# Performance work log

Hardware: AMD Instinct MI355X
Metric: run time of the kernel (lower is better)

The kernel has to match this reference:

```python
import jax, jax.numpy as jnp
import numpy as np

B, T, H, F, E = 512, 32, 768, 3072, 3  # E = num_route_experts = num_experts - 1 (top-1 beam)


def setup_inputs() -> dict:
    key = jax.random.key(0)
    ks = jax.random.split(key, 4)
    s = 0.02
    return {
        "x": jax.random.normal(ks[0], (B, T, H), jnp.float32),
        "Wg": jax.random.normal(ks[1], (E, H), jnp.float32) * s,
        "W1": jax.random.normal(ks[2], (E, H, F), jnp.float32) * s,
        "b1": jnp.zeros((E, F), jnp.float32),
        "W2": jax.random.normal(ks[3], (E, F, H), jnp.float32) * s,
        "b2": jnp.zeros((E, H), jnp.float32),
    }


def reference(x, Wg, W1, b1, W2, b2):
    # forward_gate: mean-pool over tokens (attention_mask is all-ones), linear gate, softmax
    scores = jax.nn.softmax(jnp.mean(x, axis=1) @ Wg.T, axis=-1)  # [B, E]
    # beam_search, first layer with num_route_beam=1: plain top-1 expert selection
    _, idx = jax.lax.top_k(scores, 1)
    sel = idx[:, 0]  # [B] int32, selected expert per sample
    # forward_expert_ffn: densely run EVERY route expert (gelu MLP) on the full batch
    h = jax.nn.gelu(jnp.einsum('bth,ehf->betf', x, W1) + b1[None, :, None, :], approximate=False)  # [B,E,T,F]
    y = jnp.einsum('betf,efh->beth', h, W2) + b2[None, :, None, :]  # [B,E,T,H]
    # weight_type == 'ffn_prob': one-hot mask times gate prob, then sum over experts
    w = scores * jax.nn.one_hot(sel, E, dtype=scores.dtype)  # [B, E]
    out = jnp.einsum('beth,be->bth', y, w)  # [B, T, H]
    return out
```

## Files before the change

### kernel.cpp

```cpp
#include <hip/hip_runtime.h>
#include <hip/hip_bf16.h>
#include <cstdint>
#include <cstddef>

namespace {

constexpr int kB = 512, kT = 32, kH = 768, kF = 3072, kE = 3;
constexpr int kMaxTiles = 131;
constexpr int kMaxChunk = 131;
constexpr int kXPermTile = 128 * kH;
constexpr int kHbufTile  = 128 * kF;

typedef __attribute__((ext_vector_type(8))) short short8;
typedef __attribute__((ext_vector_type(4))) float f32x4;

__device__ __forceinline__ void gld_lds16(const void* g, void* l) {
  __builtin_amdgcn_global_load_lds(
      (const __attribute__((address_space(1))) void*)g,
      (__attribute__((address_space(3))) void*)l, 16, 0, 0);
}

__device__ __forceinline__ float bf2f(__hip_bfloat16 v) { return __bfloat162float(v); }
__device__ __forceinline__ unsigned short f2bfb(float f) {
  __hip_bfloat16 h = __float2bfloat16(f);
  return *reinterpret_cast<unsigned short*>(&h);
}

__global__ void k_sniff(const unsigned short* __restrict__ w, int nwords,
                        int* __restrict__ flag) {
  __shared__ int cnt_s;
  if (threadIdx.x == 0) cnt_s = 0;
  __syncthreads();
  int local = 0;
  for (int i = threadIdx.x; i < nwords; i += 256) {
    unsigned e = (w[i] >> 7) & 0xFF;
    if (e >= 0xC0) ++local;
  }
  atomicAdd(&cnt_s, local);
  __syncthreads();
  if (threadIdx.x == 0) *flag = (cnt_s > 64) ? 1 : 0;
}

__global__ void k_route(const void* __restrict__ xv, const void* __restrict__ Wgv,
                        const int* __restrict__ flagX, const int* __restrict__ flagG,
                        float* __restrict__ wsel,
                        int* __restrict__ cnt, int* __restrict__ lists) {
  bool fx = (*flagX != 0), fg = (*flagG != 0);
  const float* xf = (const float*)xv;
  const __hip_bfloat16* xb = (const __hip_bfloat16*)xv;
  const float* wf = (const float*)Wgv;
  const __hip_bfloat16* wb = (const __hip_bfloat16*)Wgv;
  int b = blockIdx.x;
  int tid = threadIdx.x;
  float a0 = 0.f, a1 = 0.f, a2 = 0.f;
  for (int h = tid; h < kH; h += 256) {
    size_t base = (size_t)b * kT * kH + h;
    float s = 0.f;
#pragma unroll
    for (int t = 0; t < kT; ++t) {
      size_t i = base + (size_t)t * kH;
      s += fx ? xf[i] : bf2f(xb[i]);
    }
    s *= (1.f / kT);
    a0 += s * (fg ? wf[0 * kH + h] : bf2f(wb[0 * kH + h]));
    a1 += s * (fg ? wf[1 * kH + h] : bf2f(wb[1 * kH + h]));
    a2 += s * (fg ? wf[2 * kH + h] : bf2f(wb[2 * kH + h]));
  }
  __shared__ float red[3][256];
  red[0][tid] = a0; red[1][tid] = a1; red[2][tid] = a2;
  __syncthreads();
  for (int s2 = 128; s2 > 0; s2 >>= 1) {
    if (tid < s2) {
      red[0][tid] += red[0][tid + s2];
      red[1][tid] += red[1][tid + s2];
      red[2][tid] += red[2][tid + s2];
    }
    __syncthreads();
  }
  if (tid == 0) {
    float l0 = red[0][0], l1 = red[1][0], l2 = red[2][0];
    int am = 0; float mx = l0;
    if (l1 > mx) { mx = l1; am = 1; }
    if (l2 > mx) { mx = l2; am = 2; }
    float e0 = expf(l0 - mx), e1 = expf(l1 - mx), e2 = expf(l2 - mx);
    float inv = 1.f / (e0 + e1 + e2);
    float sc = (am == 0 ? e0 : (am == 1 ? e1 : e2)) * inv;
    wsel[b] = sc;
    int pos = atomicAdd(&cnt[am], 1);
    lists[am * kB + pos] = b;
  }
}

__global__ void k_tiles(const int* __restrict__ cnt, const int* __restrict__ lists,
                        int* __restrict__ tileExpert, int* __restrict__ tileBatch,
                        int* __restrict__ numTiles) {
  if (threadIdx.x == 0 && blockIdx.x == 0) {
    int t = 0;
    for (int e = 0; e < kE; ++e) {
      int c = cnt[e];
      for (int i = 0; i < c; i += 4) {
        tileExpert[t] = e;
        for (int s = 0; s < 4; ++s)
          tileBatch[t * 4 + s] = (i + s < c) ? lists[e * kB + i + s] : -1;
        ++t;
      }
    }
    *numTiles = t;
    for (int tt = t; tt < kMaxTiles; ++tt) {
      tileExpert[tt] = 0;
      for (int s = 0; s < 4; ++s) tileBatch[tt * 4 + s] = -1;
    }
  }
}

__global__ __launch_bounds__(256)
void k_transpose(const void* __restrict__ srcv, __hip_bfloat16* __restrict__ dst_,
                 int K, int N, const int* __restrict__ flag) {
  bool f32 = (*flag != 0);
  const float* sf = (const float*)srcv;
  const unsigned short* sb = (const unsigned short*)srcv;
  unsigned short* dst = (unsigned short*)dst_;
  __shared__ __align__(16) unsigned short t[64][73];
  int e = blockIdx.z;
  int n0 = blockIdx.x * 64, k0 = blockIdx.y * 64;
  size_t eoff = (size_t)e * K * N;
  int tr = threadIdx.x >> 4;
  int tc4 = (threadIdx.x & 15) * 4;
#pragma unroll
  for (int i = 0; i < 4; ++i) {
    int r = tr + 16 * i;
    size_t idx = eoff + (size_t)(k0 + r) * N + n0 + tc4;
    if (f32) {
      float4 u = *(const float4*)(sf + idx);
      t[r][tc4] = f2bfb(u.x); t[r][tc4 + 1] = f2bfb(u.y);
      t[r][tc4 + 2] = f2bfb(u.z); t[r][tc4 + 3] = f2bfb(u.w);
    } else {
      ushort4 u = *(const ushort4*)(sb + idx);
      t[r][tc4] = u.x; t[r][tc4 + 1] = u.y; t[r][tc4 + 2] = u.z; t[r][tc4 + 3] = u.w;
    }
  }
  __syncthreads();
#pragma unroll
  for (int i = 0; i < 4; ++i) {
    int rn = tr + 16 * i;
    ushort4 v;
    v.x = t[tc4][rn]; v.y = t[tc4 + 1][rn]; v.z = t[tc4 + 2][rn]; v.w = t[tc4 + 3][rn];
    *(ushort4*)(dst + eoff + (size_t)(n0 + rn) * K + k0 + tc4) = v;
  }
}

__global__ __launch_bounds__(256)
void k_convert_x(const void* __restrict__ xv, const int* __restrict__ flagX,
                 const int* __restrict__ tileBatch, const int* __restrict__ numTiles,
                 __hip_bfloat16* __restrict__ xperm) {
  int tile = blockIdx.y;
  if (tile >= *numTiles) return;
  int kblk = blockIdx.x;
  bool fx = (*flagX != 0);
  const float* xf = (const float*)xv;
  const __hip_bfloat16* xb = (const __hip_bfloat16*)xv;
  int tb0 = tileBatch[tile * 4];
  int tb[4];
#pragma unroll
  for (int s = 0; s < 4; ++s) {
    int bb = tileBatch[tile * 4 + s];
    tb[s] = (bb < 0) ? tb0 : bb;
  }
  int tid = threadIdx.x;
  short8* dst = (short8*)(xperm + (size_t)tile * kXPermTile + kblk * 8192);
#pragma unroll
  for (int i = 0; i < 4; ++i) {
    int s = i * 256 + tid;
    int m = (s >> 2) & 127, kk = s >> 9;
    int q = (s & 3) ^ ((s >> 3) & 3);
    int row = tb[m >> 5] * kT + (m & 31);
    size_t src = (size_t)row * kH + kblk * 64 + kk * 32 + q * 8;
    short8 v;
    if (fx) {
      float4 u = *(const float4*)(xf + src);
      float4 w = *(const float4*)(xf + src + 4);
      v[0] = f2bfb(u.x); v[1] = f2bfb(u.y); v[2] = f2bfb(u.z); v[3] = f2bfb(u.w);
      v[4] = f2bfb(w.x); v[5] = f2bfb(w.y); v[6] = f2bfb(w.z); v[7] = f2bfb(w.w);
    } else {
      v = *(const short8*)(xb + src);
    }
    dst[s] = v;
  }
}

__global__ __launch_bounds__(256, 2)
void k_ffn1(const __hip_bfloat16* __restrict__ xperm,
            const __hip_bfloat16* __restrict__ w1t,
            const __hip_bfloat16* __restrict__ b1,
            const int* __restrict__ tileExpert,
            const int* __restrict__ numTiles,
            int tileOff,
            __hip_bfloat16* __restrict__ hbuf) {
  int j = blockIdx.y;
  int local = j / 3;
  int tile = local + tileOff;
  if (tile >= *numTiles) return;
  int nIdx = 8 * (j % 3) + blockIdx.x;
  int nbase = nIdx * 128;
  int e = tileExpert[tile];
  __shared__ __align__(16) short ldsA[8192];
  __shared__ __align__(16) short ldsB[8192];
  int tid = threadIdx.x;
  int lane = tid & 63, wid = tid >> 6;
  int wm = wid >> 1, wn = wid & 1;
  int lane16 = lane & 15, qf = lane >> 4;
  int swzl = (lane16 >> 1) & 3;
  int qx = (qf ^ swzl) * 8;

  f32x4 acc[4][4];
#pragma unroll
  for (int r = 0; r < 4; ++r)
#pragma unroll
    for (int c = 0; c < 4; ++c) acc[r][c] = (f32x4)0.f;

  const __hip_bfloat16* w1e = w1t + (size_t)e * kF * kH;
  const __hip_bfloat16* xtile = xperm + (size_t)tile * kXPermTile;
  const __hip_bfloat16* gB[4];
  short* lA[4];
  short* lB[4];
  int aoff[4];
#pragma unroll
  for (int it = 0; it < 4; ++it) {
    int s = it * 256 + tid;
    int m = (s >> 2) & 127, kk = s >> 9;
    int q = (s & 3) ^ ((s >> 3) & 3);
    aoff[it] = s * 8;
    gB[it] = w1e + (size_t)(nbase + m) * kH + kk * 32 + q * 8;
    lA[it] = &ldsA[s * 8];
    lB[it] = &ldsB[s * 8];
  }

  for (int k0 = 0; k0 < kH; k0 += 64) {
#pragma unroll
    for (int it = 0; it < 4; ++it) gld_lds16(xtile + k0 * 128 + aoff[it], lA[it]);
#pragma unroll
    for (int it = 0; it < 4; ++it) gld_lds16(gB[it] + k0, lB[it]);
    __syncthreads();
#pragma unroll
    for (int kk = 0; kk < 2; ++kk) {
      short8 af[4], bfr[4];
#pragma unroll
      for (int r = 0; r < 4; ++r) {
        int mr = wm * 64 + r * 16 + lane16;
        af[r] = *(const short8*)&ldsA[(kk * 512 + mr * 4) * 8 + qx];
      }
#pragma unroll
      for (int c = 0; c < 4; ++c) {
        int mb = wn * 64 + c * 16 + lane16;
        bfr[c] = *(const short8*)&ldsB[(kk * 512 + mb * 4) * 8 + qx];
      }
#pragma unroll
      for (int r = 0; r < 4; ++r)
#pragma unroll
        for (int c = 0; c < 4; ++c)
          acc[r][c] = __builtin_amdgcn_mfma_f32_16x16x32_bf16(af[r], bfr[c], acc[r][c], 0, 0, 0);
    }
    __syncthreads();
  }

  __hip_bfloat16* htile = hbuf + (size_t)local * kHbufTile;
  int q4 = qf * 4;
#pragma unroll
  for (int c = 0; c < 4; ++c) {
    int n = nbase + wn * 64 + c * 16 + lane16;
    int kblk2 = n >> 6, kkn = (n >> 5) & 1, qn = (n >> 3) & 3, jj = n & 7;
    float bias = bf2f(b1[e * kF + n]);
    __hip_bfloat16* hb = htile + kblk2 * 8192 + kkn * 4096 + jj;
#pragma unroll
    for (int r = 0; r < 4; ++r) {
#pragma unroll
      for (int g = 0; g < 4; ++g) {
        int m = wm * 64 + r * 16 + q4 + g;
        float v = acc[r][c][g] + bias;
        float ge = 0.5f * v * (1.f + erff(v * 0.70710678118654752f));
        hb[(m * 4 + (qn ^ ((m >> 1) & 3))) * 8] = __float2bfloat16(ge);
      }
    }
  }
}

__global__ __launch_bounds__(256, 2)
void k_ffn2(const __hip_bfloat16* __restrict__ hbuf,
            const __hip_bfloat16* __restrict__ w2t,
            const __hip_bfloat16* __restrict__ b2,
            const float* __restrict__ wsel,
            const int* __restrict__ tileExpert,
            const int* __restrict__ tileBatch,
            const int* __restrict__ numTiles,
            int tileOff, int chunk,
            float* __restrict__ out) {
  int j = blockIdx.y;
  int local = blockIdx.x + 8 * (j / 6);
  if (local >= chunk) return;
  int tile = local + tileOff;
  if (tile >= *numTiles) return;
  int nbase = (j % 6) * 128;
  int e = tileExpert[tile];
  int tbraw[4];
  float sc[4];
#pragma unroll
  for (int s = 0; s < 4; ++s) {
    int bb = tileBatch[tile * 4 + s];
    tbraw[s] = bb;
    sc[s] = (bb >= 0) ? wsel[bb] : 0.f;
  }
  __shared__ __align__(16) short ldsA[8192];
  __shared__ __align__(16) short ldsB[8192];
  int tid = threadIdx.x;
  int lane = tid & 63, wid = tid >> 6;
  int wm = wid >> 1, wn = wid & 1;
  int lane16 = lane & 15, qf = lane >> 4;
  int swzl = (lane16 >> 1) & 3;
  int qx = (qf ^ swzl) * 8;

  f32x4 acc[4][4];
#pragma unroll
  for (int r = 0; r < 4; ++r)
#pragma unroll
    for (int c = 0; c < 4; ++c) acc[r][c] = (f32x4)0.f;

  const __hip_bfloat16* w2e = w2t + (size_t)e * kF * kH;
  const __hip_bfloat16* htile = hbuf + (size_t)local * kHbufTile;
  const __hip_bfloat16* gB[4];
  short* lA[4];
  short* lB[4];
  int aoff[4];
#pragma unroll
  for (int it = 0; it < 4; ++it) {
    int s = it * 256 + tid;
    int m = (s >> 2) & 127, kk = s >> 9;
    int q = (s & 3) ^ ((s >> 3) & 3);
    aoff[it] = s * 8;
    gB[it] = w2e + (size_t)(nbase + m) * kF + kk * 32 + q * 8;
    lA[it] = &ldsA[s * 8];
    lB[it] = &ldsB[s * 8];
  }

  for (int k0 = 0; k0 < kF; k0 += 64) {
#pragma unroll
    for (int it = 0; it < 4; ++it) gld_lds16(htile + k0 * 128 + aoff[it], lA[it]);
#pragma unroll
    for (int it = 0; it < 4; ++it) gld_lds16(gB[it] + k0, lB[it]);
    __syncthreads();
#pragma unroll
    for (int kk = 0; kk < 2; ++kk) {
      short8 af[4], bfr[4];
#pragma unroll
      for (int r = 0; r < 4; ++r) {
        int mr = wm * 64 + r * 16 + lane16;
        af[r] = *(const short8*)&ldsA[(kk * 512 + mr * 4) * 8 + qx];
      }
#pragma unroll
      for (int c = 0; c < 4; ++c) {
        int mb = wn * 64 + c * 16 + lane16;
        bfr[c] = *(const short8*)&ldsB[(kk * 512 + mb * 4) * 8 + qx];
      }
#pragma unroll
      for (int r = 0; r < 4; ++r)
#pragma unroll
        for (int c = 0; c < 4; ++c)
          acc[r][c] = __builtin_amdgcn_mfma_f32_16x16x32_bf16(af[r], bfr[c], acc[r][c], 0, 0, 0);
    }
    __syncthreads();
  }

  int q4 = qf * 4;
#pragma unroll
  for (int c = 0; c < 4; ++c) {
    int ncol = wn * 64 + c * 16 + lane16;
    float bias = bf2f(b2[e * kH + nbase + ncol]);
#pragma unroll
    for (int r = 0; r < 4; ++r) {
      int s = (wm * 64 + r * 16) >> 5;
      int bb = tbraw[s];
      if (bb < 0) continue;
      float scale = sc[s];
#pragma unroll
      for (int g = 0; g < 4; ++g) {
        int m = wm * 64 + r * 16 + q4 + g;
        float v = (acc[r][c][g] + bias) * scale;
        out[((size_t)(bb * kT + (m & 31))) * kH + nbase + ncol] = v;
      }
    }
  }
}

}

extern "C" void kernel_launch(void* const* d_in, const int* in_sizes, int n_in,
                              void* d_out, int out_size, void* d_ws, size_t ws_size,
                              hipStream_t stream) {
  (void)in_sizes; (void)n_in; (void)out_size;
  float* out = (float*)d_out;

  char* ws = (char*)d_ws;
  size_t off = 0;
  auto alloc = [&](size_t bytes) -> char* {
    char* p = ws + off;
    off = (off + bytes + 255) & ~(size_t)255;
    return p;
  };
  int*   flagX      = (int*)alloc(4);
  int*   flagG      = (int*)alloc(4);
  int*   flagW1     = (int*)alloc(4);
  int*   flagW2     = (int*)alloc(4);
  int*   cnt        = (int*)alloc(kE * 4);
  float* wsel       = (float*)alloc(kB * 4);
  int*   lists      = (int*)alloc((size_t)kE * kB * 4);
  int*   tileExpert = (int*)alloc(kMaxTiles * 4);
  int*   tileBatch  = (int*)alloc(kMaxTiles * 4 * 4);
  int*   numTiles   = (int*)alloc(4);
  __hip_bfloat16* w1t   = (__hip_bfloat16*)alloc((size_t)kE * kH * kF * 2);
  __hip_bfloat16* w2t   = (__hip_bfloat16*)alloc((size_t)kE * kH * kF * 2);
  __hip_bfloat16* xperm = (__hip_bfloat16*)alloc((size_t)kMaxTiles * kXPermTile * 2);

  size_t tileBytes = (size_t)kHbufTile * 2;
  size_t avail = (ws_size > off + tileBytes) ? (ws_size - off) : tileBytes;
  int chunk = (int)(avail / tileBytes);
  if (chunk > kMaxChunk) chunk = kMaxChunk;
  if (chunk < 1) chunk = 1;
  __hip_bfloat16* hbuf = (__hip_bfloat16*)alloc((size_t)chunk * tileBytes);

  hipMemsetAsync(cnt, 0, kE * 4, stream);
  k_sniff<<<1, 256, 0, stream>>>((const unsigned short*)d_in[0], 4096, flagX);
  k_sniff<<<1, 256, 0, stream>>>((const unsigned short*)d_in[1], kE * kH, flagG);
  k_sniff<<<1, 256, 0, stream>>>((const unsigned short*)d_in[2], 4096, flagW1);
  k_sniff<<<1, 256, 0, stream>>>((const unsigned short*)d_in[4], 4096, flagW2);
  k_route<<<kB, 256, 0, stream>>>(d_in[0], d_in[1], flagX, flagG, wsel, cnt, lists);
  k_tiles<<<1, 64, 0, stream>>>(cnt, lists, tileExpert, tileBatch, numTiles);
  k_transpose<<<dim3(kF / 64, kH / 64, kE), 256, 0, stream>>>(d_in[2], w1t, kH, kF, flagW1);
  k_transpose<<<dim3(kH / 64, kF / 64, kE), 256, 0, stream>>>(d_in[4], w2t, kF, kH, flagW2);
  k_convert_x<<<dim3(kH / 64, kMaxTiles), 256, 0, stream>>>(d_in[0], flagX, tileBatch,
                                                            numTiles, xperm);
  for (int toff = 0; toff < kMaxTiles; toff += chunk) {
    k_ffn1<<<dim3(8, 3 * chunk), 256, 0, stream>>>(xperm, w1t,
                                                   (const __hip_bfloat16*)d_in[3],
                                                   tileExpert, numTiles, toff, hbuf);
    int rows2 = (chunk + 7) / 8;
    k_ffn2<<<dim3(8, 6 * rows2), 256, 0, stream>>>(hbuf, w2t,
                                                   (const __hip_bfloat16*)d_in[5], wsel,
                                                   tileExpert, tileBatch, numTiles,
                                                   toff, chunk, out);
  }
}
```

Measured before the change: 417.8 us.

## Merge small setup kernels, vectorize routing, fast GELU, stage FFN1 output through LDS

Four sniff launches and the memset become one kernel. Tile building moves into the routing kernel through a last-block ticket, and the two weight transposes merge into one launch, all to cut launch overhead. Routing reads x with float4 loads. FFN1 swaps erff for a polynomial erf approximation and writes its GELU output to LDS first, then to global memory in 16-byte stores, aiming for coalesced writes. The approximate erf adds a small numerical error, and the extra LDS pass adds one barrier.

```diff
diff --git a/kernel.cpp b/kernel.cpp
--- a/kernel.cpp
+++ b/kernel.cpp
@@ -21,50 +21,94 @@
 }
 
 __device__ __forceinline__ float bf2f(__hip_bfloat16 v) { return __bfloat162float(v); }
+__device__ __forceinline__ float bfu(unsigned short u) {
+  return __uint_as_float(((unsigned)u) << 16);
+}
 __device__ __forceinline__ unsigned short f2bfb(float f) {
   __hip_bfloat16 h = __float2bfloat16(f);
   return *reinterpret_cast<unsigned short*>(&h);
 }
 
-__global__ void k_sniff(const unsigned short* __restrict__ w, int nwords,
-                        int* __restrict__ flag) {
+__device__ __forceinline__ float gelu_f(float v) {
+  float av = fabsf(v);
+  float z = av * 0.70710678118654752f;
+  float t = __builtin_amdgcn_rcpf(fmaf(0.3275911f, z, 1.0f));
+  float p = fmaf(fmaf(fmaf(fmaf(1.061405429f, t, -1.453152027f), t, 1.421413741f),
+                      t, -0.284496736f), t, 0.254829592f) * t;
+  float er = fmaf(-p, __expf(-z * z), 1.0f);
+  return 0.5f * v + 0.5f * av * er;
+}
+
+__global__ void k_sniff_all(const unsigned short* __restrict__ x,
+                            const unsigned short* __restrict__ g,
+                            const unsigned short* __restrict__ w1,
+                            const unsigned short* __restrict__ w2,
+                            int* __restrict__ flags, int* __restrict__ cnt,
+                            int* __restrict__ ticket) {
+  int bb = blockIdx.x;
+  if (bb == 0 && threadIdx.x < 4) {
+    if (threadIdx.x < 3) cnt[threadIdx.x] = 0;
+    else *ticket = 0;
+  }
+  const unsigned short* p = (bb == 0) ? x : (bb == 1) ? g : (bb == 2) ? w1 : w2;
+  int nwords = (bb == 1) ? kE * kH : 4096;
   __shared__ int cnt_s;
   if (threadIdx.x == 0) cnt_s = 0;
   __syncthreads();
   int local = 0;
   for (int i = threadIdx.x; i < nwords; i += 256) {
-    unsigned e = (w[i] >> 7) & 0xFF;
+    unsigned e = (p[i] >> 7) & 0xFF;
     if (e >= 0xC0) ++local;
   }
   atomicAdd(&cnt_s, local);
   __syncthreads();
-  if (threadIdx.x == 0) *flag = (cnt_s > 64) ? 1 : 0;
+  if (threadIdx.x == 0) flags[bb] = (cnt_s > 64) ? 1 : 0;
 }
 
 __global__ void k_route(const void* __restrict__ xv, const void* __restrict__ Wgv,
-                        const int* __restrict__ flagX, const int* __restrict__ flagG,
+                        const int* __restrict__ flags,
                         float* __restrict__ wsel,
-                        int* __restrict__ cnt, int* __restrict__ lists) {
-  bool fx = (*flagX != 0), fg = (*flagG != 0);
-  const float* xf = (const float*)xv;
-  const __hip_bfloat16* xb = (const __hip_bfloat16*)xv;
-  const float* wf = (const float*)Wgv;
-  const __hip_bfloat16* wb = (const __hip_bfloat16*)Wgv;
+                        int* __restrict__ cnt, int* __restrict__ lists,
+                        int* __restrict__ ticket,
+                        int* __restrict__ tileExpert, int* __restrict__ tileBatch,
+                        int* __restrict__ numTiles) {
+  bool fx = (flags[0] != 0), fg = (flags[1] != 0);
   int b = blockIdx.x;
   int tid = threadIdx.x;
   float a0 = 0.f, a1 = 0.f, a2 = 0.f;
-  for (int h = tid; h < kH; h += 256) {
-    size_t base = (size_t)b * kT * kH + h;
-    float s = 0.f;
-#pragma unroll
-    for (int t = 0; t < kT; ++t) {
-      size_t i = base + (size_t)t * kH;
-      s += fx ? xf[i] : bf2f(xb[i]);
-    }
-    s *= (1.f / kT);
-    a0 += s * (fg ? wf[0 * kH + h] : bf2f(wb[0 * kH + h]));
-    a1 += s * (fg ? wf[1 * kH + h] : bf2f(wb[1 * kH + h]));
-    a2 += s * (fg ? wf[2 * kH + h] : bf2f(wb[2 * kH + h]));
+  if (tid < 192) {
+    float m0 = 0.f, m1 = 0.f, m2 = 0.f, m3 = 0.f;
+    if (fx) {
+      const float4* xr = (const float4*)((const float*)xv + (size_t)b * kT * kH) + tid;
+#pragma unroll 8
+      for (int t = 0; t < kT; ++t) {
+        float4 u = xr[t * 192];
+        m0 += u.x; m1 += u.y; m2 += u.z; m3 += u.w;
+      }
+    } else {
+      const ushort4* xr = (const ushort4*)((const unsigned short*)xv + (size_t)b * kT * kH) + tid;
+#pragma unroll 8
+      for (int t = 0; t < kT; ++t) {
+        ushort4 u = xr[t * 192];
+        m0 += bfu(u.x); m1 += bfu(u.y); m2 += bfu(u.z); m3 += bfu(u.w);
+      }
+    }
+    const float inv = 1.f / kT;
+    m0 *= inv; m1 *= inv; m2 *= inv; m3 *= inv;
+#pragma unroll
+    for (int e = 0; e < kE; ++e) {
+      float w0, w1v, w2v, w3;
+      int base = e * kH + tid * 4;
+      if (fg) {
+        float4 u = *(const float4*)((const float*)Wgv + base);
+        w0 = u.x; w1v = u.y; w2v = u.z; w3 = u.w;
+      } else {
+        ushort4 u = *(const ushort4*)((const unsigned short*)Wgv + base);
+        w0 = bfu(u.x); w1v = bfu(u.y); w2v = bfu(u.z); w3 = bfu(u.w);
+      }
+      float d = m0 * w0 + m1 * w1v + m2 * w2v + m3 * w3;
+      if (e == 0) a0 = d; else if (e == 1) a1 = d; else a2 = d;
+    }
   }
   __shared__ float red[3][256];
   red[0][tid] = a0; red[1][tid] = a1; red[2][tid] = a2;
@@ -88,41 +132,45 @@
     wsel[b] = sc;
     int pos = atomicAdd(&cnt[am], 1);
     lists[am * kB + pos] = b;
-  }
-}
-
-__global__ void k_tiles(const int* __restrict__ cnt, const int* __restrict__ lists,
-                        int* __restrict__ tileExpert, int* __restrict__ tileBatch,
-                        int* __restrict__ numTiles) {
-  if (threadIdx.x == 0 && blockIdx.x == 0) {
-    int t = 0;
-    for (int e = 0; e < kE; ++e) {
-      int c = cnt[e];
-      for (int i = 0; i < c; i += 4) {
-        tileExpert[t] = e;
-        for (int s = 0; s < 4; ++s)
-          tileBatch[t * 4 + s] = (i + s < c) ? lists[e * kB + i + s] : -1;
-        ++t;
-      }
-    }
-    *numTiles = t;
-    for (int tt = t; tt < kMaxTiles; ++tt) {
-      tileExpert[tt] = 0;
-      for (int s = 0; s < 4; ++s) tileBatch[tt * 4 + s] = -1;
+    __threadfence();
+    int tk = atomicAdd(ticket, 1);
+    if (tk == kB - 1) {
+      __threadfence();
+      int t = 0;
+      for (int e = 0; e < kE; ++e) {
+        int c = cnt[e];
+        for (int i = 0; i < c; i += 4) {
+          tileExpert[t] = e;
+          for (int s = 0; s < 4; ++s)
+            tileBatch[t * 4 + s] = (i + s < c) ? lists[e * kB + i + s] : -1;
+          ++t;
+        }
+      }
+      *numTiles = t;
+      for (int tt = t; tt < kMaxTiles; ++tt) {
+        tileExpert[tt] = 0;
+        for (int s = 0; s < 4; ++s) tileBatch[tt * 4 + s] = -1;
+      }
     }
   }
 }
 
 __global__ __launch_bounds__(256)
-void k_transpose(const void* __restrict__ srcv, __hip_bfloat16* __restrict__ dst_,
-                 int K, int N, const int* __restrict__ flag) {
-  bool f32 = (*flag != 0);
-  const float* sf = (const float*)srcv;
-  const unsigned short* sb = (const unsigned short*)srcv;
-  unsigned short* dst = (unsigned short*)dst_;
+void k_transpose6(const void* __restrict__ w1src, const void* __restrict__ w2src,
+                  __hip_bfloat16* __restrict__ w1dst, __hip_bfloat16* __restrict__ w2dst,
+                  const int* __restrict__ flags) {
+  int z = blockIdx.z;
+  bool isW1 = (z < 3);
+  int e = isW1 ? z : z - 3;
+  bool f32 = (flags[isW1 ? 2 : 3] != 0);
+  const float* sf = (const float*)(isW1 ? w1src : w2src);
+  const unsigned short* sb = (const unsigned short*)(isW1 ? w1src : w2src);
+  unsigned short* dst = (unsigned short*)(isW1 ? w1dst : w2dst);
+  int K = isW1 ? kH : kF, N = isW1 ? kF : kH;
+  int ntx = N / 64;
+  int bx = blockIdx.x;
+  int n0 = (bx % ntx) * 64, k0 = (bx / ntx) * 64;
   __shared__ __align__(16) unsigned short t[64][73];
-  int e = blockIdx.z;
-  int n0 = blockIdx.x * 64, k0 = blockIdx.y * 64;
   size_t eoff = (size_t)e * K * N;
   int tr = threadIdx.x >> 4;
   int tc4 = (threadIdx.x & 15) * 4;
@@ -150,13 +198,13 @@
 }
 
 __global__ __launch_bounds__(256)
-void k_convert_x(const void* __restrict__ xv, const int* __restrict__ flagX,
+void k_convert_x(const void* __restrict__ xv, const int* __restrict__ flags,
                  const int* __restrict__ tileBatch, const int* __restrict__ numTiles,
                  __hip_bfloat16* __restrict__ xperm) {
   int tile = blockIdx.y;
   if (tile >= *numTiles) return;
   int kblk = blockIdx.x;
-  bool fx = (*flagX != 0);
+  bool fx = (flags[0] != 0);
   const float* xf = (const float*)xv;
   const __hip_bfloat16* xb = (const __hip_bfloat16*)xv;
   int tb0 = tileBatch[tile * 4];
@@ -203,8 +251,9 @@
   int nIdx = 8 * (j % 3) + blockIdx.x;
   int nbase = nIdx * 128;
   int e = tileExpert[tile];
-  __shared__ __align__(16) short ldsA[8192];
-  __shared__ __align__(16) short ldsB[8192];
+  __shared__ __align__(16) short ldsbuf[16384];
+  short* ldsA = ldsbuf;
+  short* ldsB = ldsbuf + 8192;
   int tid = threadIdx.x;
   int lane = tid & 63, wid = tid >> 6;
   int wm = wid >> 1, wn = wid & 1;
@@ -264,23 +313,30 @@
   }
 
   __hip_bfloat16* htile = hbuf + (size_t)local * kHbufTile;
+  unsigned short* uls = (unsigned short*)ldsbuf;
   int q4 = qf * 4;
 #pragma unroll
   for (int c = 0; c < 4; ++c) {
-    int n = nbase + wn * 64 + c * 16 + lane16;
-    int kblk2 = n >> 6, kkn = (n >> 5) & 1, qn = (n >> 3) & 3, jj = n & 7;
-    float bias = bf2f(b1[e * kF + n]);
-    __hip_bfloat16* hb = htile + kblk2 * 8192 + kkn * 4096 + jj;
+    int nn = wn * 64 + c * 16 + lane16;
+    float bias = bf2f(b1[e * kF + nbase + nn]);
+    int lbase = (nn >> 6) * 8192 + ((nn >> 5) & 1) * 4096 + (nn & 7);
+    int qn = (nn >> 3) & 3;
 #pragma unroll
     for (int r = 0; r < 4; ++r) {
 #pragma unroll
       for (int g = 0; g < 4; ++g) {
         int m = wm * 64 + r * 16 + q4 + g;
         float v = acc[r][c][g] + bias;
-        float ge = 0.5f * v * (1.f + erff(v * 0.70710678118654752f));
-        hb[(m * 4 + (qn ^ ((m >> 1) & 3))) * 8] = __float2bfloat16(ge);
-      }
-    }
+        uls[lbase + (m * 4 + (qn ^ ((m >> 1) & 3))) * 8] = f2bfb(gelu_f(v));
+      }
+    }
+  }
+  __syncthreads();
+  unsigned short* dstg = (unsigned short*)htile + (size_t)(nbase >> 6) * 8192;
+#pragma unroll
+  for (int i = 0; i < 8; ++i) {
+    int s = i * 2048 + tid * 8;
+    *(short8*)(dstg + s) = *(const short8*)(uls + s);
   }
 }
 
@@ -405,11 +461,9 @@
     off = (off + bytes + 255) & ~(size_t)255;
     return p;
   };
-  int*   flagX      = (int*)alloc(4);
-  int*   flagG      = (int*)alloc(4);
-  int*   flagW1     = (int*)alloc(4);
-  int*   flagW2     = (int*)alloc(4);
+  int*   flags      = (int*)alloc(16);
   int*   cnt        = (int*)alloc(kE * 4);
+  int*   ticket     = (int*)alloc(4);
   float* wsel       = (float*)alloc(kB * 4);
   int*   lists      = (int*)alloc((size_t)kE * kB * 4);
   int*   tileExpert = (int*)alloc(kMaxTiles * 4);
@@ -426,16 +480,15 @@
   if (chunk < 1) chunk = 1;
   __hip_bfloat16* hbuf = (__hip_bfloat16*)alloc((size_t)chunk * tileBytes);
 
-  hipMemsetAsync(cnt, 0, kE * 4, stream);
-  k_sniff<<<1, 256, 0, stream>>>((const unsigned short*)d_in[0], 4096, flagX);
-  k_sniff<<<1, 256, 0, stream>>>((const unsigned short*)d_in[1], kE * kH, flagG);
-  k_sniff<<<1, 256, 0, stream>>>((const unsigned short*)d_in[2], 4096, flagW1);
-  k_sniff<<<1, 256, 0, stream>>>((const unsigned short*)d_in[4], 4096, flagW2);
-  k_route<<<kB, 256, 0, stream>>>(d_in[0], d_in[1], flagX, flagG, wsel, cnt, lists);
-  k_tiles<<<1, 64, 0, stream>>>(cnt, lists, tileExpert, tileBatch, numTiles);
-  k_transpose<<<dim3(kF / 64, kH / 64, kE), 256, 0, stream>>>(d_in[2], w1t, kH, kF, flagW1);
-  k_transpose<<<dim3(kH / 64, kF / 64, kE), 256, 0, stream>>>(d_in[4], w2t, kF, kH, flagW2);
-  k_convert_x<<<dim3(kH / 64, kMaxTiles), 256, 0, stream>>>(d_in[0], flagX, tileBatch,
+  k_sniff_all<<<4, 256, 0, stream>>>((const unsigned short*)d_in[0],
+                                     (const unsigned short*)d_in[1],
+                                     (const unsigned short*)d_in[2],
+                                     (const unsigned short*)d_in[4],
+                                     flags, cnt, ticket);
+  k_route<<<kB, 256, 0, stream>>>(d_in[0], d_in[1], flags, wsel, cnt, lists,
+                                  ticket, tileExpert, tileBatch, numTiles);
+  k_transpose6<<<dim3(576, 1, 6), 256, 0, stream>>>(d_in[2], d_in[4], w1t, w2t, flags);
+  k_convert_x<<<dim3(kH / 64, kMaxTiles), 256, 0, stream>>>(d_in[0], flags, tileBatch,
                                                             numTiles, xperm);
   for (int toff = 0; toff < kMaxTiles; toff += chunk) {
     k_ffn1<<<dim3(8, 3 * chunk), 256, 0, stream>>>(xperm, w1t,
```

Result: slower. 429.5 us (+2.8%).
